# Kernel optimization log

Measured on AMD Instinct MI355X. Metric: run time of the kernel, lower is better.

## Reference

```python
import jax, jax.numpy as jnp
import numpy as np

D_MODEL = 1024
HEAD = 64

def setup_inputs() -> dict:
    key = jax.random.key(0)
    kx, kk, kq, kv, kbk, kbq, kbv = jax.random.split(key, 7)
    s = 1.0 / np.sqrt(D_MODEL)
    return {
        "x": jax.random.normal(kx, (4, 2048, D_MODEL), dtype=jnp.float32),
        "Wk": jax.random.uniform(kk, (D_MODEL, HEAD), minval=-s, maxval=s, dtype=jnp.float32),
        "Wq": jax.random.uniform(kq, (D_MODEL, HEAD), minval=-s, maxval=s, dtype=jnp.float32),
        "Wv": jax.random.uniform(kv, (D_MODEL, HEAD), minval=-s, maxval=s, dtype=jnp.float32),
        "bk": jax.random.uniform(kbk, (HEAD,), minval=-s, maxval=s, dtype=jnp.float32),
        "bq": jax.random.uniform(kbq, (HEAD,), minval=-s, maxval=s, dtype=jnp.float32),
        "bv": jax.random.uniform(kbv, (HEAD,), minval=-s, maxval=s, dtype=jnp.float32),
    }

def reference(x, Wk, Wq, Wv, bk, bq, bv):
    B, T, C = x.shape
    k = x @ Wk + bk  # [B,T,H]
    q = x @ Wq + bq
    v = x @ Wv + bv
    # NOTE: original scales by sqrt(C) = sqrt(d_model), not head_size
    scores = jnp.einsum('bth,bsh->bts', q, k) / jnp.sqrt(jnp.float32(C))
    causal = jnp.tril(jnp.ones((T, T), dtype=bool))
    scores = jnp.where(causal, scores, -jnp.inf)
    attn = jax.nn.softmax(scores, axis=-1)
    # dropout p=0.0 -> identity
    return jnp.einsum('bts,bsh->bth', attn, v)
```

## Files before the change

kernel.cpp:

```cpp
#include <hip/hip_runtime.h>
#include <hip/hip_bf16.h>

#define D_MODEL 1024
#define HEAD 64
#define TSEQ 2048
#define NB 4
#define BT (NB * TSEQ)

typedef __bf16 bf16x8 __attribute__((ext_vector_type(8)));
typedef __bf16 bf16x4 __attribute__((ext_vector_type(4)));
typedef float f32x4 __attribute__((ext_vector_type(4)));

#define LOG2E 1.44269504088896f

__device__ inline unsigned pkbf(float a, float b) {
    union { __bf16 h[2]; unsigned u; } t;
    t.h[0] = (__bf16)a; t.h[1] = (__bf16)b;
    return t.u;
}

__global__ __launch_bounds__(256) void wt_kernel(
    const float* __restrict__ Wq, const float* __restrict__ Wk,
    const float* __restrict__ Wv, __bf16* __restrict__ wtf)
{
    __shared__ float ws_[256][20];

    int jt = blockIdx.x >> 2;
    int chunk = blockIdx.x & 3;
    int tsel = jt >> 2;
    int colbase = (jt & 3) * 16;
    const float* W = tsel == 0 ? Wq : (tsel == 1 ? Wk : Wv);

    int t = threadIdx.x;
#pragma unroll
    for (int i = 0; i < 4; ++i) {
        int f4 = t + 256 * i;
        int krow = f4 >> 2, cg = f4 & 3;
        float4 v = *(const float4*)(W + (size_t)(chunk * 256 + krow) * 64 + colbase + cg * 4);
        *(float4*)(&ws_[krow][cg * 4]) = v;
    }
    __syncthreads();

#pragma unroll
    for (int sidx = 0; sidx < 2; ++sidx) {
        int s = t + 256 * sidx;
        int kk = s >> 6;
        int lane = s & 63;
        int c16 = lane & 15, g = lane >> 4;
        bf16x8 o;
#pragma unroll
        for (int i = 0; i < 8; ++i)
            o[i] = (__bf16)ws_[kk * 32 + g * 8 + i][c16];
        *(bf16x8*)(wtf + ((size_t)(jt * 32 + chunk * 8 + kk) * 64 + lane) * 8) = o;
    }
}

#define XPITCH 1032

__global__ __launch_bounds__(512, 4) void qkv_gemm(
    const float* __restrict__ x, const __bf16* __restrict__ wtf,
    const float* __restrict__ bq, const float* __restrict__ bk, const float* __restrict__ bv,
    __bf16* __restrict__ qs, __bf16* __restrict__ kf, __bf16* __restrict__ vf)
{
    __shared__ __align__(16) char lds_raw[49152];
    __bf16 (*xls)[XPITCH] = (__bf16(*)[XPITCH])lds_raw;
    f32x4 (*red)[6][64]   = (f32x4(*)[6][64])lds_raw;

    int d = blockIdx.x;
    int bi = d >> 3;
    int strip = (d & 7) * 64 + (bi >> 1);
    int ch = bi & 1;
    int r0 = strip * 16;

    int tid = threadIdx.x;
    int w = tid >> 6;
    int lane = tid & 63;
    int c16 = lane & 15, g = lane >> 4;

#pragma unroll
    for (int i = 0; i < 8; ++i) {
        int f4 = tid + 512 * i;
        int row = f4 >> 8;
        int k = (f4 & 255) * 4;
        float4 v = *(const float4*)(x + (size_t)(r0 + row) * D_MODEL + k);
        bf16x4 o;
        o[0] = (__bf16)v.x; o[1] = (__bf16)v.y;
        o[2] = (__bf16)v.z; o[3] = (__bf16)v.w;
        *(bf16x4*)(&xls[row][k]) = o;
    }
    __syncthreads();

    f32x4 acc[6];
#pragma unroll
    for (int j = 0; j < 6; ++j) acc[j] = (f32x4){0.f, 0.f, 0.f, 0.f};

#pragma unroll
    for (int kt = 0; kt < 4; ++kt) {
        int ktile = w * 4 + kt;
        bf16x8 af = *(const bf16x8*)(&xls[c16][ktile * 32 + g * 8]);
        const __bf16* wb = wtf + ((size_t)ktile * 64 + lane) * 8;
#pragma unroll
        for (int j = 0; j < 6; ++j) {
            bf16x8 bfr = *(const bf16x8*)(wb + (size_t)(ch * 6 + j) * 32 * 64 * 8);
            acc[j] = __builtin_amdgcn_mfma_f32_16x16x32_bf16(af, bfr, acc[j], 0, 0, 0);
        }
    }

    __syncthreads();
#pragma unroll
    for (int j = 0; j < 6; ++j) red[w][j][lane] = acc[j];
    __syncthreads();

    if (w < 6) {
        int j = w;
        f32x4 s = red[0][j][lane];
#pragma unroll
        for (int sw = 1; sw < 8; ++sw) s += red[sw][j][lane];

        int col = ch * 96 + j * 16 + c16;
        int tsel = col >> 6;
        int cm = col & 63;
        const float* bias = tsel == 0 ? bq : (tsel == 1 ? bk : bv);
        float bval = bias[cm];

        int row0 = r0 + g * 4;
        int b = row0 >> 11;
        int tloc = row0 & (TSEQ - 1);
        int ti = tloc >> 5;
        int fraghalf = (tloc >> 4) & 1;

        if (tsel == 0) {
#pragma unroll
            for (int r = 0; r < 4; ++r)
                qs[(size_t)(row0 + r) * HEAD + cm] = (__bf16)((s[r] + bval) * (0.03125f * LOG2E));
        } else if (tsel == 1) {
            int f = 2 * fraghalf + (cm >> 5);
            int gk = (cm & 31) >> 3;
            int ik = cm & 7;
            __bf16* base = kf + (((size_t)(b * 64 + ti) * 4 + f) * 64) * 8 + ik;
#pragma unroll
            for (int r = 0; r < 4; ++r)
                base[(size_t)((g * 4 + r) + 16 * gk) * 8] = (__bf16)(s[r] + bval);
        } else {
            int hh = cm >> 4;
            int gp = 2 * fraghalf + (g >> 1);
            bf16x4 o;
#pragma unroll
            for (int r = 0; r < 4; ++r) o[r] = (__bf16)(s[r] + bval);
            *(bf16x4*)(vf + (((size_t)(b * 64 + ti) * 4 + hh) * 64 + (cm & 15) + 16 * gp) * 8 + (g & 1) * 4) = o;
        }
    }
}

__global__ __launch_bounds__(512, 4) void attn_mfma(
    const __bf16* __restrict__ qs, const __bf16* __restrict__ kf,
    const __bf16* __restrict__ vf, float* __restrict__ out)
{
    __shared__ __align__(16) f32x4 ocomb[8][4][64];
    __shared__ float mcomb[8][16];
    __shared__ float lcomb[8][16];

    int d = blockIdx.x;
    int xcd = d & 7;
    int slot = d >> 3;
    int b = xcd >> 1;
    int qt = ((xcd & 1) ? 127 : 126) - 2 * slot;
    int qb = qt * 16;

    int tid = threadIdx.x;
    int w = tid >> 6;
    int lane = tid & 63;
    int g = lane >> 4;
    int c16 = lane & 15;

    const __bf16* qsb = qs + (size_t)(b * TSEQ + qb) * HEAD;
    const __bf16* kfb = kf + (size_t)(b * 64) * 4 * 512;
    const __bf16* vfb = vf + (size_t)(b * 64) * 4 * 512;

    bf16x8 qf0 = *(const bf16x8*)(qsb + c16 * HEAD + g * 8);
    bf16x8 qf1 = *(const bf16x8*)(qsb + c16 * HEAD + 32 + g * 8);

    f32x4 o0 = {0.f, 0.f, 0.f, 0.f}, o1 = o0, o2 = o0, o3 = o0;
    float m = -3.0e38f, l = 0.f;

    int nt = (qb + 47) >> 5;
    int qrow = qb + c16;

    bf16x8 k00c, k01c, k10c, k11c;
    if (w < nt) {
        const __bf16* kt_ = kfb + (size_t)w * 4 * 512 + lane * 8;
        k00c = *(const bf16x8*)(kt_);
        k01c = *(const bf16x8*)(kt_ + 512);
        k10c = *(const bf16x8*)(kt_ + 1024);
        k11c = *(const bf16x8*)(kt_ + 1536);
    }

    for (int ti = w; ti < nt; ti += 8) {
        int kbase = ti * 32;

        const __bf16* vt_ = vfb + (size_t)ti * 4 * 512 + lane * 8;
        bf16x8 v0 = *(const bf16x8*)(vt_);
        bf16x8 v1 = *(const bf16x8*)(vt_ + 512);
        bf16x8 v2 = *(const bf16x8*)(vt_ + 1024);
        bf16x8 v3 = *(const bf16x8*)(vt_ + 1536);

        bool pf = (ti + 8) < nt;
        bf16x8 k00n, k01n, k10n, k11n;
        if (pf) {
            const __bf16* kn_ = kfb + (size_t)(ti + 8) * 4 * 512 + lane * 8;
            k00n = *(const bf16x8*)(kn_);
            k01n = *(const bf16x8*)(kn_ + 512);
            k10n = *(const bf16x8*)(kn_ + 1024);
            k11n = *(const bf16x8*)(kn_ + 1536);
        }

        f32x4 z = {0.f, 0.f, 0.f, 0.f};
        f32x4 s0 = __builtin_amdgcn_mfma_f32_16x16x32_bf16(k00c, qf0, z, 0, 0, 0);
        s0 = __builtin_amdgcn_mfma_f32_16x16x32_bf16(k01c, qf1, s0, 0, 0, 0);
        f32x4 s1 = __builtin_amdgcn_mfma_f32_16x16x32_bf16(k10c, qf0, z, 0, 0, 0);
        s1 = __builtin_amdgcn_mfma_f32_16x16x32_bf16(k11c, qf1, s1, 0, 0, 0);

        if (kbase + 31 > qb) {
#pragma unroll
            for (int r = 0; r < 4; ++r) {
                if (kbase + 4 * g + r > qrow)      s0[r] = -3.0e38f;
                if (kbase + 16 + 4 * g + r > qrow) s1[r] = -3.0e38f;
            }
        }

        float vmax = fmaxf(fmaxf(fmaxf(s0[0], s0[1]), fmaxf(s0[2], s0[3])),
                           fmaxf(fmaxf(s1[0], s1[1]), fmaxf(s1[2], s1[3])));
        vmax = fmaxf(vmax, __shfl_xor(vmax, 16, 64));
        vmax = fmaxf(vmax, __shfl_xor(vmax, 32, 64));
        float mn = fmaxf(m, vmax);
        float al = exp2f(m - mn);
        m = mn;

        float p0[4], p1[4];
        float rsum = 0.f;
#pragma unroll
        for (int r = 0; r < 4; ++r) {
            p0[r] = exp2f(s0[r] - m);
            p1[r] = exp2f(s1[r] - m);
            rsum += p0[r] + p1[r];
        }
        rsum += __shfl_xor(rsum, 16, 64);
        rsum += __shfl_xor(rsum, 32, 64);
        l = l * al + rsum;
        o0 *= al; o1 *= al; o2 *= al; o3 *= al;

        unsigned pk[4];
        pk[0] = pkbf(p0[0], p0[1]); pk[1] = pkbf(p0[2], p0[3]);
        pk[2] = pkbf(p1[0], p1[1]); pk[3] = pkbf(p1[2], p1[3]);

        union { unsigned u[4]; bf16x8 v; } pb;
#pragma unroll
        for (int t = 0; t < 4; ++t) {
            int srcl = c16 + 16 * ((2 * g + (t >> 1)) & 3);
            unsigned lo = (unsigned)__shfl((int)pk[t & 1], srcl, 64);
            unsigned hi = (unsigned)__shfl((int)pk[2 + (t & 1)], srcl, 64);
            pb.u[t] = (g < 2) ? lo : hi;
        }

        o0 = __builtin_amdgcn_mfma_f32_16x16x32_bf16(v0, pb.v, o0, 0, 0, 0);
        o1 = __builtin_amdgcn_mfma_f32_16x16x32_bf16(v1, pb.v, o1, 0, 0, 0);
        o2 = __builtin_amdgcn_mfma_f32_16x16x32_bf16(v2, pb.v, o2, 0, 0, 0);
        o3 = __builtin_amdgcn_mfma_f32_16x16x32_bf16(v3, pb.v, o3, 0, 0, 0);

        if (pf) { k00c = k00n; k01c = k01n; k10c = k10n; k11c = k11n; }
    }

    ocomb[w][0][lane] = o0;
    ocomb[w][1][lane] = o1;
    ocomb[w][2][lane] = o2;
    ocomb[w][3][lane] = o3;
    if (g == 0) {
        mcomb[w][c16] = m;
        lcomb[w][c16] = l;
    }
    __syncthreads();

    if (w < 4) {
        float M = mcomb[0][c16];
#pragma unroll
        for (int sw = 1; sw < 8; ++sw) M = fmaxf(M, mcomb[sw][c16]);
        f32x4 O = {0.f, 0.f, 0.f, 0.f};
        float L = 0.f;
#pragma unroll
        for (int sw = 0; sw < 8; ++sw) {
            float e = exp2f(mcomb[sw][c16] - M);
            L += lcomb[sw][c16] * e;
            f32x4 po = ocomb[sw][w][lane];
            O[0] += po[0] * e; O[1] += po[1] * e;
            O[2] += po[2] * e; O[3] += po[3] * e;
        }
        float rcp = 1.0f / L;
        f32x4 res = {O[0] * rcp, O[1] * rcp, O[2] * rcp, O[3] * rcp};
        *(f32x4*)(out + (size_t)(b * TSEQ + qb + c16) * HEAD + w * 16 + g * 4) = res;
    }
}

extern "C" void kernel_launch(void* const* d_in, const int* in_sizes, int n_in,
                              void* d_out, int out_size, void* d_ws, size_t ws_size,
                              hipStream_t stream) {
    const float* x  = (const float*)d_in[0];
    const float* Wk = (const float*)d_in[1];
    const float* Wq = (const float*)d_in[2];
    const float* Wv = (const float*)d_in[3];
    const float* bk = (const float*)d_in[4];
    const float* bq = (const float*)d_in[5];
    const float* bv = (const float*)d_in[6];
    float* out = (float*)d_out;

    __bf16* qs  = (__bf16*)d_ws;
    __bf16* kf  = qs + (size_t)BT * HEAD;
    __bf16* vf  = kf + (size_t)BT * HEAD;
    __bf16* wtf = vf + (size_t)BT * HEAD;

    wt_kernel<<<48, 256, 0, stream>>>(Wq, Wk, Wv, wtf);
    qkv_gemm<<<1024, 512, 0, stream>>>(x, wtf, bq, bk, bv, qs, kf, vf);
    attn_mfma<<<512, 512, 0, stream>>>(qs, kf, vf, out);
}
```

Measured before the change: 36.33 us.

## Retile QKV GEMM to 32-row blocks with per-wave full-K output tiles

The QKV projection kernel now gives each block 32 rows of x and all 192 output columns, where before each block had 16 rows and half the columns. Each wave computes a 16x48 tile over the full K dimension, so the cross-wave split-K reduction through LDS and its extra barriers are gone. Each block loads x once instead of twice, cutting redundant global reads of x. In exchange the grid drops from 1024 to 256 blocks and occupancy falls (launch bounds 4 to 2, larger LDS), so latency hiding and parallelism may suffer.

```diff
diff --git a/kernel.cpp b/kernel.cpp
--- a/kernel.cpp
+++ b/kernel.cpp
@@ -57,28 +57,26 @@
 
 #define XPITCH 1032
 
-__global__ __launch_bounds__(512, 4) void qkv_gemm(
+__global__ __launch_bounds__(512, 2) void qkv_gemm(
     const float* __restrict__ x, const __bf16* __restrict__ wtf,
     const float* __restrict__ bq, const float* __restrict__ bk, const float* __restrict__ bv,
     __bf16* __restrict__ qs, __bf16* __restrict__ kf, __bf16* __restrict__ vf)
 {
-    __shared__ __align__(16) char lds_raw[49152];
-    __bf16 (*xls)[XPITCH] = (__bf16(*)[XPITCH])lds_raw;
-    f32x4 (*red)[6][64]   = (f32x4(*)[6][64])lds_raw;
+    __shared__ __align__(16) __bf16 xls[32][XPITCH];
 
     int d = blockIdx.x;
-    int bi = d >> 3;
-    int strip = (d & 7) * 64 + (bi >> 1);
-    int ch = bi & 1;
-    int r0 = strip * 16;
+    int strip = (d & 7) * 32 + (d >> 3);
+    int r0 = strip * 32;
 
     int tid = threadIdx.x;
     int w = tid >> 6;
+    int rt = w >> 2;
+    int cq = w & 3;
     int lane = tid & 63;
     int c16 = lane & 15, g = lane >> 4;
 
 #pragma unroll
-    for (int i = 0; i < 8; ++i) {
+    for (int i = 0; i < 16; ++i) {
         int f4 = tid + 512 * i;
         int row = f4 >> 8;
         int k = (f4 & 255) * 4;
@@ -90,44 +88,37 @@
     }
     __syncthreads();
 
-    f32x4 acc[6];
-#pragma unroll
-    for (int j = 0; j < 6; ++j) acc[j] = (f32x4){0.f, 0.f, 0.f, 0.f};
-
-#pragma unroll
-    for (int kt = 0; kt < 4; ++kt) {
-        int ktile = w * 4 + kt;
-        bf16x8 af = *(const bf16x8*)(&xls[c16][ktile * 32 + g * 8]);
-        const __bf16* wb = wtf + ((size_t)ktile * 64 + lane) * 8;
-#pragma unroll
-        for (int j = 0; j < 6; ++j) {
-            bf16x8 bfr = *(const bf16x8*)(wb + (size_t)(ch * 6 + j) * 32 * 64 * 8);
+    f32x4 acc[3];
+#pragma unroll
+    for (int j = 0; j < 3; ++j) acc[j] = (f32x4){0.f, 0.f, 0.f, 0.f};
+
+    int arow = rt * 16 + c16;
+    int jt0 = cq * 3;
+
+#pragma unroll 8
+    for (int kt = 0; kt < 32; ++kt) {
+        bf16x8 af = *(const bf16x8*)(&xls[arow][kt * 32 + g * 8]);
+#pragma unroll
+        for (int j = 0; j < 3; ++j) {
+            bf16x8 bfr = *(const bf16x8*)(wtf + ((size_t)((jt0 + j) * 32 + kt) * 64 + lane) * 8);
             acc[j] = __builtin_amdgcn_mfma_f32_16x16x32_bf16(af, bfr, acc[j], 0, 0, 0);
         }
     }
 
-    __syncthreads();
-#pragma unroll
-    for (int j = 0; j < 6; ++j) red[w][j][lane] = acc[j];
-    __syncthreads();
-
-    if (w < 6) {
-        int j = w;
-        f32x4 s = red[0][j][lane];
-#pragma unroll
-        for (int sw = 1; sw < 8; ++sw) s += red[sw][j][lane];
-
-        int col = ch * 96 + j * 16 + c16;
-        int tsel = col >> 6;
-        int cm = col & 63;
+    int row0 = r0 + rt * 16 + g * 4;
+    int b = row0 >> 11;
+    int tloc = row0 & (TSEQ - 1);
+    int ti = tloc >> 5;
+    int fraghalf = (tloc >> 4) & 1;
+
+#pragma unroll
+    for (int j = 0; j < 3; ++j) {
+        int jt = jt0 + j;
+        int tsel = jt >> 2;
+        int cm = (jt & 3) * 16 + c16;
         const float* bias = tsel == 0 ? bq : (tsel == 1 ? bk : bv);
         float bval = bias[cm];
-
-        int row0 = r0 + g * 4;
-        int b = row0 >> 11;
-        int tloc = row0 & (TSEQ - 1);
-        int ti = tloc >> 5;
-        int fraghalf = (tloc >> 4) & 1;
+        f32x4 s = acc[j];
 
         if (tsel == 0) {
 #pragma unroll
@@ -318,6 +309,6 @@
     __bf16* wtf = vf + (size_t)BT * HEAD;
 
     wt_kernel<<<48, 256, 0, stream>>>(Wq, Wk, Wv, wtf);
-    qkv_gemm<<<1024, 512, 0, stream>>>(x, wtf, bq, bk, bv, qs, kf, vf);
+    qkv_gemm<<<256, 512, 0, stream>>>(x, wtf, bq, bk, bv, qs, kf, vf);
     attn_mfma<<<512, 512, 0, stream>>>(qs, kf, vf, out);
 }
```

Measured after the change: 40.78 us. 1.12x slower.
